# Optimization experiments

Measured on AMD Instinct MI355X. Metric: run time of the kernel, lower is better.

Reference implementation:

```python
import jax, jax.numpy as jnp
import numpy as np

D_MODEL = 1024
NUM_HEADS = 16
D_K = D_MODEL // NUM_HEADS
D_FF = 4096
EPS = 1e-5


def layer_norm(x, gamma, beta):
    mu = jnp.mean(x, axis=-1, keepdims=True)
    var = jnp.mean(jnp.square(x - mu), axis=-1, keepdims=True)
    return (x - mu) * jax.lax.rsqrt(var + EPS) * gamma + beta


def setup_inputs() -> dict:
    key = jax.random.key(0)
    ks = jax.random.split(key, 12)
    B, S = 2, 2048
    s_attn = 1.0 / np.sqrt(D_MODEL)
    s_ff1 = 1.0 / np.sqrt(D_MODEL)
    s_ff2 = 1.0 / np.sqrt(D_FF)
    return {
        "x": jax.random.normal(ks[0], (B, S, D_MODEL), dtype=jnp.float32),
        "mask": jnp.ones((B, 1, 1, S), dtype=jnp.int32),
        "Wq": jax.random.normal(ks[1], (D_MODEL, D_MODEL), jnp.float32) * s_attn,
        "bq": jnp.zeros((D_MODEL,), jnp.float32),
        "Wk": jax.random.normal(ks[2], (D_MODEL, D_MODEL), jnp.float32) * s_attn,
        "bk": jnp.zeros((D_MODEL,), jnp.float32),
        "Wv": jax.random.normal(ks[3], (D_MODEL, D_MODEL), jnp.float32) * s_attn,
        "bv": jnp.zeros((D_MODEL,), jnp.float32),
        "Wo": jax.random.normal(ks[4], (D_MODEL, D_MODEL), jnp.float32) * s_attn,
        "bo": jnp.zeros((D_MODEL,), jnp.float32),
        "W1": jax.random.normal(ks[5], (D_MODEL, D_FF), jnp.float32) * s_ff1,
        "b1": jnp.zeros((D_FF,), jnp.float32),
        "W2": jax.random.normal(ks[6], (D_FF, D_MODEL), jnp.float32) * s_ff2,
        "b2": jnp.zeros((D_MODEL,), jnp.float32),
        "g1": jnp.ones((D_MODEL,), jnp.float32),
        "be1": jnp.zeros((D_MODEL,), jnp.float32),
        "g2": jnp.ones((D_MODEL,), jnp.float32),
        "be2": jnp.zeros((D_MODEL,), jnp.float32),
    }


def reference(x, mask, Wq, bq, Wk, bk, Wv, bv, Wo, bo, W1, b1, W2, b2, g1, be1, g2, be2):
    B, S, _ = x.shape

    def split_heads(t):  # [B,S,D] -> [B,H,S,Dk]
        return t.reshape(B, S, NUM_HEADS, D_K).transpose(0, 2, 1, 3)

    q = split_heads(x @ Wq + bq)
    k = split_heads(x @ Wk + bk)
    v = split_heads(x @ Wv + bv)

    scores = jnp.einsum("bhsd,bhtd->bhst", q, k) / np.sqrt(D_K)
    scores = jnp.where(mask == 0, -jnp.inf, scores)
    probs = jax.nn.softmax(scores, axis=-1)
    attn = jnp.einsum("bhst,bhtd->bhsd", probs, v)
    attn = attn.transpose(0, 2, 1, 3).reshape(B, S, D_MODEL)
    attn_out = attn @ Wo + bo

    h = layer_norm(x + attn_out, g1, be1)  # dropout=0 (eval)
    ff = jax.nn.relu(h @ W1 + b1) @ W2 + b2
    out = layer_norm(h + ff, g2, be2)
    return out
```

## Files before the change

### kernel.cpp

```cpp
#include <hip/hip_runtime.h>
#include <hip/hip_bf16.h>

#define DMODEL 1024
#define DFF    4096
#define NHEAD  16
#define DK     64
#define SEQ    2048
#define BATCH  2
#define MTOT   (BATCH*SEQ)
#define LOG2E  1.44269504f
#define MREF_L2E (-14.0f * 1.44269504f)

typedef __attribute__((ext_vector_type(8))) short bf16x8;
typedef __attribute__((ext_vector_type(4))) float f32x4;

typedef const unsigned int __attribute__((address_space(1)))* gas_u32p;
typedef unsigned int __attribute__((address_space(3)))* las_u32p;

__device__ __forceinline__ void gload_lds16(const void* g, void* l) {
  __builtin_amdgcn_global_load_lds((gas_u32p)g, (las_u32p)l, 16, 0, 0);
}

__device__ __forceinline__ f32x4 mfma16(bf16x8 a, bf16x8 b, f32x4 c) {
  return __builtin_amdgcn_mfma_f32_16x16x32_bf16(a, b, c, 0, 0, 0);
}

__device__ __forceinline__ unsigned short bf16bits(float f) {
  union { __hip_bfloat16 h; unsigned short u; } c; c.h = __float2bfloat16(f); return c.u;
}

__device__ __forceinline__ unsigned pack_bf16(float a, float b) {
  return (unsigned)bf16bits(a) | ((unsigned)bf16bits(b) << 16);
}

__device__ __forceinline__ void store_bf16x4(__hip_bfloat16* p, float a, float b, float c, float d) {
  union { __hip_bfloat16 h[4]; ushort4 u; } pk;
  pk.h[0] = __float2bfloat16(a); pk.h[1] = __float2bfloat16(b);
  pk.h[2] = __float2bfloat16(c); pk.h[3] = __float2bfloat16(d);
  *(ushort4*)p = pk.u;
}

__global__ __launch_bounds__(256) void cvt_bf16_kernel(const float* __restrict__ in,
                                                       __hip_bfloat16* __restrict__ out, int n) {
  int i = (blockIdx.x * 256 + threadIdx.x) * 4;
  if (i >= n) return;
  float4 v = *(const float4*)(in + i);
  store_bf16x4(out + i, v.x, v.y, v.z, v.w);
}

__global__ __launch_bounds__(256) void transpose_cvt_kernel(const float* __restrict__ in,
                                                            __hip_bfloat16* __restrict__ out,
                                                            int R, int C) {
  __shared__ float tile[32][33];
  int tx = threadIdx.x, ty = threadIdx.y;
  int c0 = blockIdx.x * 32, r0 = blockIdx.y * 32;
  #pragma unroll
  for (int j = 0; j < 32; j += 8)
    tile[ty + j][tx] = in[(size_t)(r0 + ty + j) * C + c0 + tx];
  __syncthreads();
  #pragma unroll
  for (int j = 0; j < 32; j += 8)
    out[(size_t)(c0 + ty + j) * R + r0 + tx] = __float2bfloat16(tile[tx][ty + j]);
}

__global__ __launch_bounds__(256)
void transpose4_cvt_kernel(const float* __restrict__ A0, const float* __restrict__ A1,
                           const float* __restrict__ A2, const float* __restrict__ A3,
                           __hip_bfloat16* __restrict__ O0, __hip_bfloat16* __restrict__ O1,
                           __hip_bfloat16* __restrict__ O2, __hip_bfloat16* __restrict__ O3) {
  const float* in; __hip_bfloat16* out;
  switch (blockIdx.z) {
    case 0: in = A0; out = O0; break;
    case 1: in = A1; out = O1; break;
    case 2: in = A2; out = O2; break;
    default: in = A3; out = O3; break;
  }
  __shared__ float tile[32][33];
  int tx = threadIdx.x, ty = threadIdx.y;
  int c0 = blockIdx.x * 32, r0 = blockIdx.y * 32;
  #pragma unroll
  for (int j = 0; j < 32; j += 8)
    tile[ty + j][tx] = in[(size_t)(r0 + ty + j) * DMODEL + c0 + tx];
  __syncthreads();
  #pragma unroll
  for (int j = 0; j < 32; j += 8)
    out[(size_t)(c0 + ty + j) * DMODEL + r0 + tx] = __float2bfloat16(tile[tx][ty + j]);
}

template<int MI, int NT>
__device__ __forceinline__ void gemm_core(const __hip_bfloat16* __restrict__ A,
                                          const __hip_bfloat16* __restrict__ Bt,
                                          int K, size_t blockM, size_t blockN,
                                          __hip_bfloat16* As, __hip_bfloat16* Bs,
                                          f32x4 (&acc)[MI][4]) {
  constexpr int BM = (NT / 128) * MI * 16;
  constexpr int RP = NT / 8;
  const int tid = threadIdx.x;
  const int w = tid >> 6, l = tid & 63;
  const int q = l >> 4, ln = l & 15;
  const int m_off = (w >> 1) * MI * 16, n_off = (w & 1) * 64;
  const int lr = l >> 3, lc = (l & 7) ^ lr;

  for (int k0 = 0; k0 < K; k0 += 64) {
    __syncthreads();
    #pragma unroll
    for (int t = 0; t < 128 / RP; ++t) {
      int ra = t * RP + w * 8;
      gload_lds16(Bt + (blockN + ra + lr) * (size_t)K + k0 + lc * 8, Bs + ra * 64);
      if (t < BM / RP)
        gload_lds16(A + (blockM + ra + lr) * (size_t)K + k0 + lc * 8, As + ra * 64);
    }
    __syncthreads();
    #pragma unroll
    for (int kk = 0; kk < 2; ++kk) {
      bf16x8 af[MI], bfr[4];
      #pragma unroll
      for (int mi = 0; mi < MI; ++mi) {
        int R = m_off + mi * 16 + ln;
        int p = (kk * 4 + q) ^ (R & 7);
        af[mi] = *(const bf16x8*)(As + R * 64 + p * 8);
      }
      #pragma unroll
      for (int ni = 0; ni < 4; ++ni) {
        int R = n_off + ni * 16 + ln;
        int p = (kk * 4 + q) ^ (R & 7);
        bfr[ni] = *(const bf16x8*)(Bs + R * 64 + p * 8);
      }
      #pragma unroll
      for (int mi = 0; mi < MI; ++mi)
        #pragma unroll
        for (int ni = 0; ni < 4; ++ni)
          acc[mi][ni] = mfma16(af[mi], bfr[ni], acc[mi][ni]);
    }
  }
}

template<int MI, int NT, int RELU, int WRITE_BF16>
__global__ __launch_bounds__(NT)
void gemm_bt_kernel(const __hip_bfloat16* __restrict__ A, const __hip_bfloat16* __restrict__ Bt,
                    const float* __restrict__ bias, float* __restrict__ Cf,
                    __hip_bfloat16* __restrict__ Cb, int M, int N, int K) {
  constexpr int BM = (NT / 128) * MI * 16;
  __shared__ __align__(16) __hip_bfloat16 As[BM * 64];
  __shared__ __align__(16) __hip_bfloat16 Bs[128 * 64];
  f32x4 acc[MI][4] = {};
  const size_t blockM = blockIdx.y * (size_t)BM, blockN = blockIdx.x * 128;
  gemm_core<MI, NT>(A, Bt, K, blockM, blockN, As, Bs, acc);

  const int tid = threadIdx.x;
  const int w = tid >> 6, l = tid & 63, q = l >> 4, ln = l & 15;
  const int m_off = (w >> 1) * MI * 16, n_off = (w & 1) * 64;
  #pragma unroll
  for (int ni = 0; ni < 4; ++ni) {
    size_t col = blockN + n_off + ni * 16 + ln;
    float bv = bias[col];
    #pragma unroll
    for (int mi = 0; mi < MI; ++mi) {
      size_t rowb = blockM + m_off + mi * 16 + q * 4;
      f32x4 v = acc[mi][ni];
      #pragma unroll
      for (int r = 0; r < 4; ++r) {
        float y = v[r] + bv;
        if (RELU) y = fmaxf(y, 0.0f);
        if (WRITE_BF16) Cb[(rowb + r) * N + col] = __float2bfloat16(y);
        else            Cf[(rowb + r) * N + col] = y;
      }
    }
  }
}

__global__ __launch_bounds__(256)
void gemm_qkv_kernel(const __hip_bfloat16* __restrict__ A, const __hip_bfloat16* __restrict__ Bt,
                     const float* __restrict__ bq, const float* __restrict__ bk,
                     const float* __restrict__ bv,
                     __hip_bfloat16* __restrict__ Qo, __hip_bfloat16* __restrict__ Ko,
                     __hip_bfloat16* __restrict__ VTo) {
  __shared__ __align__(16) __hip_bfloat16 As[128 * 64];
  __shared__ __align__(16) __hip_bfloat16 Bs[128 * 64];
  f32x4 acc[4][4] = {};
  const size_t blockM = blockIdx.y * 128, blockN = blockIdx.x * 128;
  const int sel = blockIdx.x >> 3;
  gemm_core<4, 256>(A, Bt, DMODEL, blockM, blockN, As, Bs, acc);

  const int tid = threadIdx.x;
  const int w = tid >> 6, l = tid & 63, q = l >> 4, ln = l & 15;
  const int m_off = (w >> 1) * 64, n_off = (w & 1) * 64;
  const int ncol0 = (int)blockN - sel * DMODEL;

  if (sel == 2) {
    #pragma unroll
    for (int ni = 0; ni < 4; ++ni) {
      int col = ncol0 + n_off + ni * 16 + ln;
      float bvv = bv[col];
      int hh = col >> 6, d = col & 63;
      #pragma unroll
      for (int mi = 0; mi < 4; ++mi) {
        size_t rowb = blockM + m_off + mi * 16 + q * 4;
        int bb = (int)(rowb >> 11), s = (int)(rowb & 2047);
        int sp = (s & ~0x1C) | ((s & 0x0C) << 1) | ((s & 0x10) >> 2);
        f32x4 v = acc[mi][ni];
        uint2 pk;
        pk.x = pack_bf16(v[0] + bvv, v[1] + bvv);
        pk.y = pack_bf16(v[2] + bvv, v[3] + bvv);
        *(uint2*)(VTo + (((size_t)(bb * NHEAD + hh) * DK + d) * SEQ + sp)) = pk;
      }
    }
  } else {
    const float* bias = (sel == 0) ? bq : bk;
    const float scale = (sel == 0) ? 0.125f : 1.0f;
    __hip_bfloat16* outp = (sel == 0) ? Qo : Ko;
    #pragma unroll
    for (int ni = 0; ni < 4; ++ni) {
      int col = ncol0 + n_off + ni * 16 + ln;
      float bvv = bias[col];
      #pragma unroll
      for (int mi = 0; mi < 4; ++mi) {
        size_t rowb = blockM + m_off + mi * 16 + q * 4;
        f32x4 v = acc[mi][ni];
        #pragma unroll
        for (int r = 0; r < 4; ++r)
          outp[(rowb + r) * DMODEL + col] = __float2bfloat16((v[r] + bvv) * scale);
      }
    }
  }
}

__global__ __launch_bounds__(128, 3)
void attn_kernel(const __hip_bfloat16* __restrict__ Q, const __hip_bfloat16* __restrict__ Kg,
                 const __hip_bfloat16* __restrict__ VT, const int* __restrict__ mask,
                 __hip_bfloat16* __restrict__ Oout) {
  const int tid = threadIdx.x, w = tid >> 6, l = tid & 63, q = l >> 4, ln = l & 15;
  const int qt = blockIdx.x, h = blockIdx.y, b = blockIdx.z;
  const size_t wrow = (size_t)b * SEQ + qt * 64 + w * 32;
  const int hcol = h * DK;
  const __hip_bfloat16* vth = VT + ((size_t)(b * NHEAD + h)) * DK * SEQ;
  const __hip_bfloat16* kgb = Kg + (size_t)b * SEQ * DMODEL + hcol;
  const int* mk = mask + (size_t)b * SEQ;

  __shared__ __align__(16) __hip_bfloat16 Ks[2][64 * 64];

  const int lr = l >> 3, lc = (l & 7) ^ lr;
  auto stage_k = [&](int buf, int kt) {
    #pragma unroll
    for (int t = 0; t < 4; ++t) {
      int ra = t * 16 + w * 8;
      gload_lds16(kgb + (size_t)(kt + ra + lr) * DMODEL + lc * 8, &Ks[buf][ra * 64]);
    }
  };

  bf16x8 qf[2][2];
  #pragma unroll
  for (int mi = 0; mi < 2; ++mi)
    #pragma unroll
    for (int kc = 0; kc < 2; ++kc)
      qf[mi][kc] = *(const bf16x8*)(Q + (wrow + mi * 16 + ln) * DMODEL + hcol + kc * 32 + q * 8);

  f32x4 Oacc[2][4] = {};
  float l_[2] = {0.f, 0.f};

  stage_k(0, 0);

  for (int it = 0; it < SEQ / 64; ++it) {
    const int kt = it * 64;
    __syncthreads();
    if (it + 1 < SEQ / 64) stage_k((it + 1) & 1, kt + 64);

    bf16x8 vf[8];
    #pragma unroll
    for (int ni = 0; ni < 4; ++ni)
      #pragma unroll
      for (int kc = 0; kc < 2; ++kc)
        vf[ni * 2 + kc] = *(const bf16x8*)(vth + (size_t)(ni * 16 + ln) * SEQ + kt + kc * 32 + q * 8);
    f32x4 mb[4];
    #pragma unroll
    for (int t = 0; t < 4; ++t) {
      int4 mv = *(const int4*)(mk + kt + t * 16 + q * 4);
      mb[t][0] = mv.x ? MREF_L2E : -1e30f; mb[t][1] = mv.y ? MREF_L2E : -1e30f;
      mb[t][2] = mv.z ? MREF_L2E : -1e30f; mb[t][3] = mv.w ? MREF_L2E : -1e30f;
    }

    const __hip_bfloat16* kb = &Ks[it & 1][0];
    f32x4 st[2][4] = {};
    #pragma unroll
    for (int kc = 0; kc < 2; ++kc)
      #pragma unroll
      for (int t = 0; t < 4; ++t) {
        int R = t * 16 + ln;
        bf16x8 kf = *(const bf16x8*)(kb + R * 64 + (((kc * 4 + q) ^ (R & 7)) << 3));
        #pragma unroll
        for (int mi = 0; mi < 2; ++mi)
          st[mi][t] = mfma16(kf, qf[mi][kc], st[mi][t]);
      }

    bf16x8 pf[2][2];
    #pragma unroll
    for (int mi = 0; mi < 2; ++mi) {
      float rs = 0.f;
      unsigned pk_[4][2];
      #pragma unroll
      for (int t = 0; t < 4; ++t) {
        float p0 = __builtin_amdgcn_exp2f(__builtin_fmaf(st[mi][t][0], LOG2E, mb[t][0]));
        float p1 = __builtin_amdgcn_exp2f(__builtin_fmaf(st[mi][t][1], LOG2E, mb[t][1]));
        float p2 = __builtin_amdgcn_exp2f(__builtin_fmaf(st[mi][t][2], LOG2E, mb[t][2]));
        float p3 = __builtin_amdgcn_exp2f(__builtin_fmaf(st[mi][t][3], LOG2E, mb[t][3]));
        rs += (p0 + p1) + (p2 + p3);
        pk_[t][0] = pack_bf16(p0, p1);
        pk_[t][1] = pack_bf16(p2, p3);
      }
      l_[mi] += rs;
      #pragma unroll
      for (int kc = 0; kc < 2; ++kc) {
        union { bf16x8 v; unsigned u[4]; } f;
        f.u[0] = pk_[kc * 2][0];     f.u[1] = pk_[kc * 2][1];
        f.u[2] = pk_[kc * 2 + 1][0]; f.u[3] = pk_[kc * 2 + 1][1];
        pf[mi][kc] = f.v;
      }
    }

    #pragma unroll
    for (int kc = 0; kc < 2; ++kc)
      #pragma unroll
      for (int mi = 0; mi < 2; ++mi)
        #pragma unroll
        for (int ni = 0; ni < 4; ++ni)
          Oacc[mi][ni] = mfma16(pf[mi][kc], vf[ni * 2 + kc], Oacc[mi][ni]);
  }

  #pragma unroll
  for (int mi = 0; mi < 2; ++mi) {
    l_[mi] += __shfl_xor(l_[mi], 16);
    l_[mi] += __shfl_xor(l_[mi], 32);
  }
  #pragma unroll
  for (int mi = 0; mi < 2; ++mi) {
    float inv = 1.0f / l_[mi];
    f32x4 i4;
    #pragma unroll
    for (int r = 0; r < 4; ++r) i4[r] = __shfl(inv, (l & 48) + q * 4 + r);
    #pragma unroll
    for (int ni = 0; ni < 4; ++ni)
      #pragma unroll
      for (int r = 0; r < 4; ++r)
        Oout[(wrow + mi * 16 + q * 4 + r) * DMODEL + hcol + ni * 16 + ln] =
            __float2bfloat16(Oacc[mi][ni][r] * i4[r]);
  }
}

__global__ __launch_bounds__(256)
void add_ln_kernel(const float* __restrict__ X, const float* __restrict__ Y,
                   const float* __restrict__ gam, const float* __restrict__ bet,
                   float* __restrict__ Of, __hip_bfloat16* __restrict__ Ob) {
  int row = blockIdx.x, tid = threadIdx.x;
  const float4 a = *(const float4*)(X + (size_t)row * DMODEL + tid * 4);
  const float4 c = *(const float4*)(Y + (size_t)row * DMODEL + tid * 4);
  float v0 = a.x + c.x, v1 = a.y + c.y, v2 = a.z + c.z, v3 = a.w + c.w;
  float s  = v0 + v1 + v2 + v3;
  float s2 = v0 * v0 + v1 * v1 + v2 * v2 + v3 * v3;
  #pragma unroll
  for (int off = 1; off < 64; off <<= 1) {
    s  += __shfl_xor(s, off);
    s2 += __shfl_xor(s2, off);
  }
  __shared__ float red[8];
  int w = tid >> 6, l = tid & 63;
  if (l == 0) { red[w] = s; red[4 + w] = s2; }
  __syncthreads();
  float S1 = red[0] + red[1] + red[2] + red[3];
  float S2 = red[4] + red[5] + red[6] + red[7];
  float mu = S1 * (1.0f / DMODEL);
  float var = S2 * (1.0f / DMODEL) - mu * mu;
  float rstd = rsqrtf(var + 1e-5f);
  const float4 gv = *(const float4*)(gam + tid * 4);
  const float4 bv = *(const float4*)(bet + tid * 4);
  float y0 = (v0 - mu) * rstd * gv.x + bv.x;
  float y1 = (v1 - mu) * rstd * gv.y + bv.y;
  float y2 = (v2 - mu) * rstd * gv.z + bv.z;
  float y3 = (v3 - mu) * rstd * gv.w + bv.w;
  float4 ov = {y0, y1, y2, y3};
  *(float4*)(Of + (size_t)row * DMODEL + tid * 4) = ov;
  if (Ob) store_bf16x4(Ob + (size_t)row * DMODEL + tid * 4, y0, y1, y2, y3);
}

extern "C" void kernel_launch(void* const* d_in, const int* in_sizes, int n_in,
                              void* d_out, int out_size, void* d_ws, size_t ws_size,
                              hipStream_t stream) {
  const float* x    = (const float*)d_in[0];
  const int*   mask = (const int*)d_in[1];
  const float* Wq = (const float*)d_in[2];  const float* bq = (const float*)d_in[3];
  const float* Wk = (const float*)d_in[4];  const float* bk = (const float*)d_in[5];
  const float* Wv = (const float*)d_in[6];  const float* bv = (const float*)d_in[7];
  const float* Wo = (const float*)d_in[8];  const float* bo = (const float*)d_in[9];
  const float* W1 = (const float*)d_in[10]; const float* b1 = (const float*)d_in[11];
  const float* W2 = (const float*)d_in[12]; const float* b2 = (const float*)d_in[13];
  const float* g1 = (const float*)d_in[14]; const float* be1 = (const float*)d_in[15];
  const float* g2 = (const float*)d_in[16]; const float* be2 = (const float*)d_in[17];
  float* out = (float*)d_out;

  char* ws = (char*)d_ws;
  const size_t MB = 1024ull * 1024ull;
  __hip_bfloat16* xb   = (__hip_bfloat16*)(ws + 0 * MB);
  __hip_bfloat16* WqT  = (__hip_bfloat16*)(ws + 8 * MB);
  __hip_bfloat16* WkT  = (__hip_bfloat16*)(ws + 10 * MB);
  __hip_bfloat16* WvT  = (__hip_bfloat16*)(ws + 12 * MB);
  __hip_bfloat16* WoT  = (__hip_bfloat16*)(ws + 14 * MB);
  __hip_bfloat16* W1T  = (__hip_bfloat16*)(ws + 16 * MB);
  __hip_bfloat16* W2T  = (__hip_bfloat16*)(ws + 24 * MB);
  __hip_bfloat16* Qb   = (__hip_bfloat16*)(ws + 32 * MB);
  __hip_bfloat16* Kb   = (__hip_bfloat16*)(ws + 40 * MB);
  __hip_bfloat16* VTb  = (__hip_bfloat16*)(ws + 48 * MB);
  __hip_bfloat16* attnB= (__hip_bfloat16*)(ws + 56 * MB);
  float*          AO   = (float*)(ws + 32 * MB);
  float*          hbuf = (float*)(ws + 48 * MB);
  __hip_bfloat16* hb   = (__hip_bfloat16*)(ws + 64 * MB);
  __hip_bfloat16* ff1  = (__hip_bfloat16*)(ws + 72 * MB);
  float*          ff2  = (float*)(ws + 32 * MB);

  dim3 blk256(256), blk128(128);
  dim3 blkT(32, 8);

  cvt_bf16_kernel<<<dim3(4096), blk256, 0, stream>>>(x, xb, MTOT * DMODEL);
  transpose4_cvt_kernel<<<dim3(32, 32, 4), blkT, 0, stream>>>(Wq, Wk, Wv, Wo, WqT, WkT, WvT, WoT);
  transpose_cvt_kernel<<<dim3(128, 32), blkT, 0, stream>>>(W1, W1T, DMODEL, DFF);
  transpose_cvt_kernel<<<dim3(32, 128), blkT, 0, stream>>>(W2, W2T, DFF, DMODEL);

  gemm_qkv_kernel<<<dim3(24, 32), blk256, 0, stream>>>(xb, WqT, bq, bk, bv, Qb, Kb, VTb);

  attn_kernel<<<dim3(32, 16, 2), blk128, 0, stream>>>(Qb, Kb, VTb, mask, attnB);

  gemm_bt_kernel<2, 256, 0, 0><<<dim3(8, 64), blk256, 0, stream>>>(attnB, WoT, bo, AO, nullptr, MTOT, DMODEL, DMODEL);

  add_ln_kernel<<<dim3(MTOT), blk256, 0, stream>>>(x, AO, g1, be1, hbuf, hb);

  gemm_bt_kernel<4, 256, 1, 1><<<dim3(32, 32), blk256, 0, stream>>>(hb, W1T, b1, nullptr, ff1, MTOT, DFF, DMODEL);

  gemm_bt_kernel<2, 256, 0, 0><<<dim3(8, 64), blk256, 0, stream>>>(ff1, W2T, b2, ff2, nullptr, MTOT, DMODEL, DFF);

  add_ln_kernel<<<dim3(MTOT), blk256, 0, stream>>>(hbuf, ff2, g2, be2, out, nullptr);
}
```

Before: 402.1 us.

## Split-K the FF2 GEMM and software-pipeline QK^T in attention

The second FFN GEMM (K=4096) is split into two K halves run as separate blocks along grid z. Each half writes fp32 partials to its own buffer, and the following add+layernorm kernel sums both partials and adds the bias. This doubles the block count to fill more CUs, at the cost of extra partial-buffer traffic. The attention loop is also restructured to process two K tiles per iteration, issuing the QK^T MFMAs for the next tile before the softmax/PV of the current one so that math and latency overlap, at the cost of more registers.

```diff
diff --git a/kernel.cpp b/kernel.cpp
--- a/kernel.cpp
+++ b/kernel.cpp
@@ -90,7 +90,7 @@
 template<int MI, int NT>
 __device__ __forceinline__ void gemm_core(const __hip_bfloat16* __restrict__ A,
                                           const __hip_bfloat16* __restrict__ Bt,
-                                          int K, size_t blockM, size_t blockN,
+                                          int Kc, int Kst, size_t blockM, size_t blockN,
                                           __hip_bfloat16* As, __hip_bfloat16* Bs,
                                           f32x4 (&acc)[MI][4]) {
   constexpr int BM = (NT / 128) * MI * 16;
@@ -101,14 +101,14 @@
   const int m_off = (w >> 1) * MI * 16, n_off = (w & 1) * 64;
   const int lr = l >> 3, lc = (l & 7) ^ lr;
 
-  for (int k0 = 0; k0 < K; k0 += 64) {
+  for (int k0 = 0; k0 < Kc; k0 += 64) {
     __syncthreads();
     #pragma unroll
     for (int t = 0; t < 128 / RP; ++t) {
       int ra = t * RP + w * 8;
-      gload_lds16(Bt + (blockN + ra + lr) * (size_t)K + k0 + lc * 8, Bs + ra * 64);
+      gload_lds16(Bt + (blockN + ra + lr) * (size_t)Kst + k0 + lc * 8, Bs + ra * 64);
       if (t < BM / RP)
-        gload_lds16(A + (blockM + ra + lr) * (size_t)K + k0 + lc * 8, As + ra * 64);
+        gload_lds16(A + (blockM + ra + lr) * (size_t)Kst + k0 + lc * 8, As + ra * 64);
     }
     __syncthreads();
     #pragma unroll
@@ -145,7 +145,7 @@
   __shared__ __align__(16) __hip_bfloat16 Bs[128 * 64];
   f32x4 acc[MI][4] = {};
   const size_t blockM = blockIdx.y * (size_t)BM, blockN = blockIdx.x * 128;
-  gemm_core<MI, NT>(A, Bt, K, blockM, blockN, As, Bs, acc);
+  gemm_core<MI, NT>(A, Bt, K, K, blockM, blockN, As, Bs, acc);
 
   const int tid = threadIdx.x;
   const int w = tid >> 6, l = tid & 63, q = l >> 4, ln = l & 15;
@@ -165,6 +165,38 @@
         if (WRITE_BF16) Cb[(rowb + r) * N + col] = __float2bfloat16(y);
         else            Cf[(rowb + r) * N + col] = y;
       }
+    }
+  }
+}
+
+template<int MI, int NT>
+__global__ __launch_bounds__(NT)
+void gemm_part_kernel(const __hip_bfloat16* __restrict__ A, const __hip_bfloat16* __restrict__ Bt,
+                      float* __restrict__ C0, float* __restrict__ C1,
+                      int M, int N, int Kc, int Kst) {
+  constexpr int BM = (NT / 128) * MI * 16;
+  __shared__ __align__(16) __hip_bfloat16 As[BM * 64];
+  __shared__ __align__(16) __hip_bfloat16 Bs[128 * 64];
+  f32x4 acc[MI][4] = {};
+  const size_t blockM = blockIdx.y * (size_t)BM, blockN = blockIdx.x * 128;
+  const __hip_bfloat16* Az  = A  + (size_t)blockIdx.z * Kc;
+  const __hip_bfloat16* Btz = Bt + (size_t)blockIdx.z * Kc;
+  gemm_core<MI, NT>(Az, Btz, Kc, Kst, blockM, blockN, As, Bs, acc);
+
+  float* C = blockIdx.z ? C1 : C0;
+  const int tid = threadIdx.x;
+  const int w = tid >> 6, l = tid & 63, q = l >> 4, ln = l & 15;
+  const int m_off = (w >> 1) * MI * 16, n_off = (w & 1) * 64;
+  #pragma unroll
+  for (int ni = 0; ni < 4; ++ni) {
+    size_t col = blockN + n_off + ni * 16 + ln;
+    #pragma unroll
+    for (int mi = 0; mi < MI; ++mi) {
+      size_t rowb = blockM + m_off + mi * 16 + q * 4;
+      f32x4 v = acc[mi][ni];
+      #pragma unroll
+      for (int r = 0; r < 4; ++r)
+        C[(rowb + r) * N + col] = v[r];
     }
   }
 }
@@ -180,7 +212,7 @@
   f32x4 acc[4][4] = {};
   const size_t blockM = blockIdx.y * 128, blockN = blockIdx.x * 128;
   const int sel = blockIdx.x >> 3;
-  gemm_core<4, 256>(A, Bt, DMODEL, blockM, blockN, As, Bs, acc);
+  gemm_core<4, 256>(A, Bt, DMODEL, DMODEL, blockM, blockN, As, Bs, acc);
 
   const int tid = threadIdx.x;
   const int w = tid >> 6, l = tid & 63, q = l >> 4, ln = l & 15;
@@ -258,29 +290,8 @@
   f32x4 Oacc[2][4] = {};
   float l_[2] = {0.f, 0.f};
 
-  stage_k(0, 0);
-
-  for (int it = 0; it < SEQ / 64; ++it) {
-    const int kt = it * 64;
-    __syncthreads();
-    if (it + 1 < SEQ / 64) stage_k((it + 1) & 1, kt + 64);
-
-    bf16x8 vf[8];
-    #pragma unroll
-    for (int ni = 0; ni < 4; ++ni)
-      #pragma unroll
-      for (int kc = 0; kc < 2; ++kc)
-        vf[ni * 2 + kc] = *(const bf16x8*)(vth + (size_t)(ni * 16 + ln) * SEQ + kt + kc * 32 + q * 8);
-    f32x4 mb[4];
-    #pragma unroll
-    for (int t = 0; t < 4; ++t) {
-      int4 mv = *(const int4*)(mk + kt + t * 16 + q * 4);
-      mb[t][0] = mv.x ? MREF_L2E : -1e30f; mb[t][1] = mv.y ? MREF_L2E : -1e30f;
-      mb[t][2] = mv.z ? MREF_L2E : -1e30f; mb[t][3] = mv.w ? MREF_L2E : -1e30f;
-    }
-
-    const __hip_bfloat16* kb = &Ks[it & 1][0];
-    f32x4 st[2][4] = {};
+  auto qkt = [&](int buf, f32x4 (&st)[2][4]) {
+    const __hip_bfloat16* kb = &Ks[buf][0];
     #pragma unroll
     for (int kc = 0; kc < 2; ++kc)
       #pragma unroll
@@ -291,7 +302,24 @@
         for (int mi = 0; mi < 2; ++mi)
           st[mi][t] = mfma16(kf, qf[mi][kc], st[mi][t]);
       }
-
+  };
+
+  auto load_v = [&](int kt, bf16x8 (&vf)[8]) {
+    #pragma unroll
+    for (int ni = 0; ni < 4; ++ni)
+      #pragma unroll
+      for (int kc = 0; kc < 2; ++kc)
+        vf[ni * 2 + kc] = *(const bf16x8*)(vth + (size_t)(ni * 16 + ln) * SEQ + kt + kc * 32 + q * 8);
+  };
+  auto load_mb = [&](int kt, f32x4 (&mb)[4]) {
+    #pragma unroll
+    for (int t = 0; t < 4; ++t) {
+      int4 mv = *(const int4*)(mk + kt + t * 16 + q * 4);
+      mb[t][0] = mv.x ? MREF_L2E : -1e30f; mb[t][1] = mv.y ? MREF_L2E : -1e30f;
+      mb[t][2] = mv.z ? MREF_L2E : -1e30f; mb[t][3] = mv.w ? MREF_L2E : -1e30f;
+    }
+  };
+  auto soft_pv = [&](f32x4 (&st)[2][4], f32x4 (&mb)[4], bf16x8 (&vf)[8]) {
     bf16x8 pf[2][2];
     #pragma unroll
     for (int mi = 0; mi < 2; ++mi) {
@@ -316,7 +344,6 @@
         pf[mi][kc] = f.v;
       }
     }
-
     #pragma unroll
     for (int kc = 0; kc < 2; ++kc)
       #pragma unroll
@@ -324,6 +351,38 @@
         #pragma unroll
         for (int ni = 0; ni < 4; ++ni)
           Oacc[mi][ni] = mfma16(pf[mi][kc], vf[ni * 2 + kc], Oacc[mi][ni]);
+  };
+
+  stage_k(0, 0);
+  __syncthreads();
+  stage_k(1, 64);
+  f32x4 stA[2][4] = {};
+  qkt(0, stA);
+
+  for (int j = 0; j < SEQ / 128; ++j) {
+    const int kt0 = j * 128, kt1 = kt0 + 64;
+
+    __syncthreads();
+    if (kt0 + 128 < SEQ) stage_k(0, kt0 + 128);
+    bf16x8 vf0[8]; f32x4 mb0[4];
+    load_v(kt0, vf0); load_mb(kt0, mb0);
+    f32x4 stB[2][4] = {};
+    qkt(1, stB);
+    soft_pv(stA, mb0, vf0);
+
+    __syncthreads();
+    if (kt1 + 128 < SEQ) stage_k(1, kt1 + 128);
+    bf16x8 vf1[8]; f32x4 mb1[4];
+    load_v(kt1, vf1); load_mb(kt1, mb1);
+    if (j + 1 < SEQ / 128) {
+      #pragma unroll
+      for (int mi = 0; mi < 2; ++mi)
+        #pragma unroll
+        for (int t = 0; t < 4; ++t)
+          stA[mi][t] = (f32x4){0.f, 0.f, 0.f, 0.f};
+      qkt(0, stA);
+    }
+    soft_pv(stB, mb1, vf1);
   }
 
   #pragma unroll
@@ -348,12 +407,21 @@
 
 __global__ __launch_bounds__(256)
 void add_ln_kernel(const float* __restrict__ X, const float* __restrict__ Y,
+                   const float* __restrict__ Y1, const float* __restrict__ bias,
                    const float* __restrict__ gam, const float* __restrict__ bet,
                    float* __restrict__ Of, __hip_bfloat16* __restrict__ Ob) {
   int row = blockIdx.x, tid = threadIdx.x;
   const float4 a = *(const float4*)(X + (size_t)row * DMODEL + tid * 4);
   const float4 c = *(const float4*)(Y + (size_t)row * DMODEL + tid * 4);
   float v0 = a.x + c.x, v1 = a.y + c.y, v2 = a.z + c.z, v3 = a.w + c.w;
+  if (Y1) {
+    const float4 d = *(const float4*)(Y1 + (size_t)row * DMODEL + tid * 4);
+    v0 += d.x; v1 += d.y; v2 += d.z; v3 += d.w;
+  }
+  if (bias) {
+    const float4 e = *(const float4*)(bias + tid * 4);
+    v0 += e.x; v1 += e.y; v2 += e.z; v3 += e.w;
+  }
   float s  = v0 + v1 + v2 + v3;
   float s2 = v0 * v0 + v1 * v1 + v2 * v2 + v3 * v3;
   #pragma unroll
@@ -413,7 +481,8 @@
   float*          hbuf = (float*)(ws + 48 * MB);
   __hip_bfloat16* hb   = (__hip_bfloat16*)(ws + 64 * MB);
   __hip_bfloat16* ff1  = (__hip_bfloat16*)(ws + 72 * MB);
-  float*          ff2  = (float*)(ws + 32 * MB);
+  float*          ff2a = (float*)(ws + 0 * MB);
+  float*          ff2b = (float*)(ws + 32 * MB);
 
   dim3 blk256(256), blk128(128);
   dim3 blkT(32, 8);
@@ -429,11 +498,11 @@
 
   gemm_bt_kernel<2, 256, 0, 0><<<dim3(8, 64), blk256, 0, stream>>>(attnB, WoT, bo, AO, nullptr, MTOT, DMODEL, DMODEL);
 
-  add_ln_kernel<<<dim3(MTOT), blk256, 0, stream>>>(x, AO, g1, be1, hbuf, hb);
+  add_ln_kernel<<<dim3(MTOT), blk256, 0, stream>>>(x, AO, nullptr, nullptr, g1, be1, hbuf, hb);
 
   gemm_bt_kernel<4, 256, 1, 1><<<dim3(32, 32), blk256, 0, stream>>>(hb, W1T, b1, nullptr, ff1, MTOT, DFF, DMODEL);
 
-  gemm_bt_kernel<2, 256, 0, 0><<<dim3(8, 64), blk256, 0, stream>>>(ff1, W2T, b2, ff2, nullptr, MTOT, DMODEL, DFF);
-
-  add_ln_kernel<<<dim3(MTOT), blk256, 0, stream>>>(hbuf, ff2, g2, be2, out, nullptr);
-}
+  gemm_part_kernel<2, 256><<<dim3(8, 64, 2), blk256, 0, stream>>>(ff1, W2T, ff2a, ff2b, MTOT, DMODEL, DFF / 2, DFF);
+
+  add_ln_kernel<<<dim3(MTOT), blk256, 0, stream>>>(hbuf, ff2a, ff2b, b2, g2, be2, out, nullptr);
+}
```

Measured after the change: 470.2 us. 1.17x slower.
